# Kernel optimization log

Measured on AMD Instinct MI355X. Metric: run time of the kernel, lower is better.

The kernel has to match this reference:

```python
import jax, jax.numpy as jnp
import numpy as np

N = 200000
K = 16
D = 32
IN_SIZE = K * (K - 1) // 2  # 120
HID = 128


def setup_inputs() -> dict:
    key = jax.random.key(0)
    ks = jax.random.split(key, 12)
    E = N * K
    x = jax.random.normal(ks[0], (N, D), dtype=jnp.float32)
    edge_attr = jax.random.normal(ks[1], (E, D), dtype=jnp.float32)
    # kNN-style edge_index: source node i owns edges [i*K, (i+1)*K)
    src = jnp.repeat(jnp.arange(N, dtype=jnp.int64), K)
    dst = jax.random.randint(ks[2], (E,), 0, N, dtype=jnp.int64)
    edge_index = jnp.stack([src, dst], axis=0)
    s = 0.1
    W1 = jax.random.normal(ks[3], (IN_SIZE, HID), dtype=jnp.float32) * s
    b1 = jnp.zeros((HID,), dtype=jnp.float32)
    W2 = jax.random.normal(ks[4], (HID, HID), dtype=jnp.float32) * s
    b2 = jnp.zeros((HID,), dtype=jnp.float32)
    W3 = jax.random.normal(ks[5], (HID, HID), dtype=jnp.float32) * s
    b3 = jnp.zeros((HID,), dtype=jnp.float32)
    W4 = jax.random.normal(ks[6], (HID, 1), dtype=jnp.float32) * s
    b4 = jnp.zeros((1,), dtype=jnp.float32)
    return {"x": x, "edge_index": edge_index, "edge_attr": edge_attr, "k": K,
            "W1": W1, "b1": b1, "W2": W2, "b2": b2, "W3": W3, "b3": b3,
            "W4": W4, "b4": b4}


def calc_pair_angles(edge_attr, k):
    # edge_attr: [N*k, d] per-edge neighbor vectors, grouped k per node
    E, d = edge_attr.shape
    n = E // k
    v = edge_attr.reshape(n, k, d)
    vn = v / (jnp.linalg.norm(v, axis=-1, keepdims=True) + 1e-12)
    cos = jnp.einsum('nkd,nmd->nkm', vn, vn)  # [n, k, k]
    cos = jnp.clip(cos, -1.0 + 1e-7, 1.0 - 1e-7)
    ang = jnp.arccos(cos)
    iu, ju = jnp.triu_indices(k, 1)
    return ang[:, iu, ju]  # [n, k*(k-1)/2]


def reference(x, edge_index, edge_attr, k, W1, b1, W2, b2, W3, b3, W4, b4):
    # message() returns edge_attr; aggregate() computes pairwise neighbor angles
    feats = calc_pair_angles(edge_attr, k)  # [N, 120]
    h = jnp.tanh(feats @ W1 + b1)
    h = jnp.tanh(h @ W2 + b2)
    h = jnp.tanh(h @ W3 + b3)
    out = jax.nn.sigmoid(h @ W4 + b4)  # [N, 1]
    return out[:, 0]  # squeeze, [N]
```

## Files before the change

kernel.cpp:

```cpp
#include <hip/hip_runtime.h>
#include <hip/hip_bf16.h>
#include <math.h>


#define NTHREADS 256
#define CHUNK    16
#define ASTRIDE  136
#define PBLOCKS  768

typedef _Float16 f16;
typedef f16  f16x8 __attribute__((ext_vector_type(8)));
typedef f16  f16x4 __attribute__((ext_vector_type(4)));
typedef float f32x4 __attribute__((ext_vector_type(4)));

#define MFMA16(a, b, c) __builtin_amdgcn_mfma_f32_16x16x32_f16(a, b, c, 0, 0, 0)

__device__ __forceinline__ float fast_tanh(float x) {
    float e = __expf(2.0f * x);
    return 1.0f - 2.0f * __builtin_amdgcn_rcpf(e + 1.0f);
}

__device__ __forceinline__ float fast_acos(float x) {
    float ax = fabsf(x);
    float p = fmaf(-0.0187293f, ax, 0.0742610f);
    p = fmaf(p, ax, -0.2121144f);
    p = fmaf(p, ax, 1.5707288f);
    float r = sqrtf(1.0f - ax) * p;
    return (x >= 0.0f) ? r : (3.14159265358979f - r);
}

__device__ __forceinline__ void load_lds16(const float* g, float* l) {
    __builtin_amdgcn_global_load_lds(
        (__attribute__((address_space(1))) void*)(g),
        (__attribute__((address_space(3))) void*)(l), 16, 0, 0);
}

__global__ void prep_weights(const float* __restrict__ W1,
                             const float* __restrict__ W2,
                             const float* __restrict__ W3,
                             f16* __restrict__ wt)
{
    int tid = blockIdx.x * 256 + threadIdx.x;
    if (tid >= 3 * 128 * 128) return;
    int layer = tid >> 14;
    int rem   = tid & 16383;
    int j     = rem >> 7;
    int i     = rem & 127;
    const float* W = (layer == 0) ? W1 : ((layer == 1) ? W2 : W3);
    int in_l = (layer == 0) ? 120 : 128;
    float v = (i < in_l) ? W[i * 128 + j] : 0.0f;
    wt[tid] = (f16)v;
}

__global__ __launch_bounds__(NTHREADS, 3)
void gnn_pipe(const float* __restrict__ edge_attr,
              const f16*   __restrict__ wt,
              const float* __restrict__ b1, const float* __restrict__ b2,
              const float* __restrict__ b3,
              const float* __restrict__ W4, const float* __restrict__ b4,
              float* __restrict__ out, int n_nodes, int nchunks)
{
    __shared__ __attribute__((aligned(16))) float stg[8192];
    __shared__ __attribute__((aligned(16))) f16   actA[16 * ASTRIDE];
    __shared__ __attribute__((aligned(16))) f16   actB[16 * ASTRIDE];
    __shared__ __attribute__((aligned(16))) float diag[4][4][16];
    __shared__ __attribute__((aligned(16))) float pbuf[16][4];
    __shared__ __attribute__((aligned(16))) float cbuf[512];

    const int t  = threadIdx.x;
    const int w  = t >> 6;
    const int l  = t & 63;
    const int lr = l & 15;
    const int lg = l >> 4;

    if (t < 128) {
        cbuf[t]       = b1[t];
        cbuf[128 + t] = b2[t];
        cbuf[256 + t] = b3[t];
        cbuf[384 + t] = W4[t];
        actA[(t >> 3) * ASTRIDE + 120 + (t & 7)] = (f16)0.f;
    }
    const float bb4 = b4[0];

    #define LW(L, jj, kt) (*(const f16x8*)(wt + (L) * 16384 + ((w * 2 + (jj)) * 16 + lr) * 128 + (kt) * 32 + lg * 8))
    const f16x8 W000 = LW(0,0,0), W001 = LW(0,0,1), W002 = LW(0,0,2), W003 = LW(0,0,3);
    const f16x8 W010 = LW(0,1,0), W011 = LW(0,1,1), W012 = LW(0,1,2), W013 = LW(0,1,3);
    const f16x8 W100 = LW(1,0,0), W101 = LW(1,0,1), W102 = LW(1,0,2), W103 = LW(1,0,3);
    const f16x8 W110 = LW(1,1,0), W111 = LW(1,1,1), W112 = LW(1,1,2), W113 = LW(1,1,3);
    const f16x8 W200 = LW(2,0,0), W201 = LW(2,0,1), W202 = LW(2,0,2), W203 = LW(2,0,3);
    const f16x8 W210 = LW(2,1,0), W211 = LW(2,1,1), W212 = LW(2,1,2), W213 = LW(2,1,3);
    #undef LW

    const int swsrc = (l * 16) ^ ((l >> 3) << 4);

    #define STAGE(ch_)                                                           \
        {                                                                        \
            const long n0_ = (long)(ch_) * CHUNK + w * 4;                        \
            _Pragma("unroll")                                                    \
            for (int i_ = 0; i_ < 8; ++i_) {                                     \
                long nd_ = n0_ + (i_ >> 1);                                      \
                if (nd_ >= n_nodes) nd_ = n_nodes - 1;                           \
                const float* gs_ = (const float*)((const char*)edge_attr         \
                                   + nd_ * 2048 + (i_ & 1) * 1024 + swsrc);      \
                load_lds16(gs_, &stg[w * 2048 + i_ * 256]);                      \
            }                                                                    \
        }

    #define LBAR()                                                               \
        {                                                                        \
            asm volatile("s_waitcnt lgkmcnt(0)" ::: "memory");                   \
            __builtin_amdgcn_s_barrier();                                        \
            __builtin_amdgcn_sched_barrier(0);                                   \
        }

    #define LAYER(SRC, DST, Wa0, Wa1, Wa2, Wa3, Wb0, Wb1, Wb2, Wb3, BOFF)       \
        {                                                                        \
            const f32x4 BV0 = *(const f32x4*)&cbuf[(BOFF) + (w * 2 + 0) * 16 + lg * 4]; \
            const f32x4 BV1 = *(const f32x4*)&cbuf[(BOFF) + (w * 2 + 1) * 16 + lg * 4]; \
            const f16* sr_ = SRC + lr * ASTRIDE + lg * 8;                        \
            f16x8 s0_ = *(const f16x8*)(sr_);                                    \
            f16x8 s1_ = *(const f16x8*)(sr_ + 32);                               \
            f16x8 s2_ = *(const f16x8*)(sr_ + 64);                               \
            f16x8 s3_ = *(const f16x8*)(sr_ + 96);                               \
            f32x4 a0_ = {0.f, 0.f, 0.f, 0.f}, a1_ = a0_;                         \
            a0_ = MFMA16(Wa0, s0_, a0_); a1_ = MFMA16(Wb0, s0_, a1_);            \
            a0_ = MFMA16(Wa1, s1_, a0_); a1_ = MFMA16(Wb1, s1_, a1_);            \
            a0_ = MFMA16(Wa2, s2_, a0_); a1_ = MFMA16(Wb2, s2_, a1_);            \
            a0_ = MFMA16(Wa3, s3_, a0_); a1_ = MFMA16(Wb3, s3_, a1_);            \
            f16x4 o0_, o1_;                                                      \
            _Pragma("unroll")                                                    \
            for (int r_ = 0; r_ < 4; ++r_) {                                     \
                o0_[r_] = (f16)fast_tanh(a0_[r_] + BV0[r_]);                     \
                o1_[r_] = (f16)fast_tanh(a1_[r_] + BV1[r_]);                     \
            }                                                                    \
            *(f16x4*)(DST + lr * ASTRIDE + (w * 2 + 0) * 16 + lg * 4) = o0_;     \
            *(f16x4*)(DST + lr * ASTRIDE + (w * 2 + 1) * 16 + lg * 4) = o1_;     \
        }

    #define LAYER3(SRC)                                                          \
        {                                                                        \
            const f32x4 bvc0 = *(const f32x4*)&cbuf[256 + (w * 2 + 0) * 16 + lg * 4]; \
            const f32x4 bvc1 = *(const f32x4*)&cbuf[256 + (w * 2 + 1) * 16 + lg * 4]; \
            const f32x4 w4v0 = *(const f32x4*)&cbuf[384 + w * 32 + lg * 4];      \
            const f32x4 w4v1 = *(const f32x4*)&cbuf[384 + w * 32 + 16 + lg * 4]; \
            const f16* sr_ = (SRC) + lr * ASTRIDE + lg * 8;                      \
            f16x8 s0_ = *(const f16x8*)(sr_);                                    \
            f16x8 s1_ = *(const f16x8*)(sr_ + 32);                               \
            f16x8 s2_ = *(const f16x8*)(sr_ + 64);                               \
            f16x8 s3_ = *(const f16x8*)(sr_ + 96);                               \
            f32x4 a0_ = {0.f, 0.f, 0.f, 0.f}, a1_ = a0_;                         \
            a0_ = MFMA16(W200, s0_, a0_); a1_ = MFMA16(W210, s0_, a1_);          \
            a0_ = MFMA16(W201, s1_, a0_); a1_ = MFMA16(W211, s1_, a1_);          \
            a0_ = MFMA16(W202, s2_, a0_); a1_ = MFMA16(W212, s2_, a1_);          \
            a0_ = MFMA16(W203, s3_, a0_); a1_ = MFMA16(W213, s3_, a1_);          \
            float p_ = 0.f;                                                      \
            _Pragma("unroll")                                                    \
            for (int r_ = 0; r_ < 4; ++r_) {                                     \
                p_ = fmaf(fast_tanh(a0_[r_] + bvc0[r_]), w4v0[r_], p_);          \
                p_ = fmaf(fast_tanh(a1_[r_] + bvc1[r_]), w4v1[r_], p_);          \
            }                                                                    \
            p_ += __shfl_xor(p_, 16);                                            \
            p_ += __shfl_xor(p_, 32);                                            \
            if (l < 16) pbuf[lr][w] = p_;                                        \
        }

    #define FINALSUM(ch_)                                                        \
        {                                                                        \
            if (l < 4) {                                                         \
                const int nd_ = w * 4 + l;                                       \
                f32x4 pv_ = *(const f32x4*)&pbuf[nd_][0];                        \
                float s_ = (pv_[0] + pv_[1]) + (pv_[2] + pv_[3]);                \
                const long gn_ = (long)(ch_) * CHUNK + nd_;                      \
                if (gn_ < n_nodes)                                               \
                    out[gn_] = __builtin_amdgcn_rcpf(1.0f + __expf(-(s_ + bb4)));\
            }                                                                    \
        }

    long ch = blockIdx.x;
    STAGE(ch);
    asm volatile("s_waitcnt vmcnt(0)" ::: "memory");
    __builtin_amdgcn_sched_barrier(0);

    int it = 0;
    for (; ch < nchunks; ch += PBLOCKS, ++it) {
        if (it) {
            asm volatile("s_waitcnt vmcnt(1)" ::: "memory");
            __builtin_amdgcn_sched_barrier(0);
        }

        const char* ws_ = (const char*)&stg[w * 2048];
        const int abase = lr * 128 + lg * 32;
        const int akey  = (lr & 7) << 4;
        f16x8 f0, f1, f2, f3;
        #define FRAG(fc, m_)                                                     \
            {                                                                    \
                float4 va = *(const float4*)(ws_ + (m_) * 2048 + (abase ^ akey));        \
                float4 vb = *(const float4*)(ws_ + (m_) * 2048 + ((abase + 16) ^ akey)); \
                fc[0]=(f16)va.x; fc[1]=(f16)va.y; fc[2]=(f16)va.z; fc[3]=(f16)va.w;      \
                fc[4]=(f16)vb.x; fc[5]=(f16)vb.y; fc[6]=(f16)vb.z; fc[7]=(f16)vb.w;      \
            }
        FRAG(f0, 0) FRAG(f1, 1) FRAG(f2, 2) FRAG(f3, 3)
        #undef FRAG

        asm volatile("s_waitcnt lgkmcnt(0)" ::: "memory");
        __builtin_amdgcn_sched_barrier(0);

        const long nxt = ch + PBLOCKS;
        if (nxt < nchunks) STAGE(nxt);

        f32x4 g0, g1, g2, g3;
        {
            f32x4 z = {0.f, 0.f, 0.f, 0.f};
            g0 = MFMA16(f0, f0, z); g1 = MFMA16(f1, f1, z);
            g2 = MFMA16(f2, f2, z); g3 = MFMA16(f3, f3, z);
        }
        if (lg == (lr >> 2)) {
            const int r = lr & 3;
            diag[w][0][lr] = __builtin_amdgcn_rsqf(g0[r] + 1e-24f);
            diag[w][1][lr] = __builtin_amdgcn_rsqf(g1[r] + 1e-24f);
            diag[w][2][lr] = __builtin_amdgcn_rsqf(g2[r] + 1e-24f);
            diag[w][3][lr] = __builtin_amdgcn_rsqf(g3[r] + 1e-24f);
        }
        asm volatile("s_waitcnt lgkmcnt(0)" ::: "memory");
        __builtin_amdgcn_sched_barrier(0);

        #define FIN(gc, c)                                                       \
            {                                                                    \
                const float rc = diag[w][c][lr];                                 \
                const f32x4 rr = *(const f32x4*)&diag[w][c][lg * 4];             \
                const int m_ = w * 4 + (c);                                      \
                const int col = lr;                                              \
                _Pragma("unroll")                                                \
                for (int r2 = 0; r2 < 4; ++r2) {                                 \
                    const int row = lg * 4 + r2;                                 \
                    float cv = gc[r2] * rr[r2] * rc;                             \
                    cv = fminf(fmaxf(cv, -1.0f + 1e-7f), 1.0f - 1e-7f);          \
                    float ang = fast_acos(cv);                                   \
                    if (row < col) {                                             \
                        const int p = 15*row - ((row*(row-1))>>1) + (col-row-1); \
                        actA[m_ * ASTRIDE + p] = (f16)ang;                       \
                    }                                                            \
                }                                                                \
            }
        FIN(g0, 0) FIN(g1, 1) FIN(g2, 2) FIN(g3, 3)
        #undef FIN

        LBAR();

        LAYER(actA, actB, W000, W001, W002, W003, W010, W011, W012, W013, 0);
        LBAR();
        LAYER(actB, actA, W100, W101, W102, W103, W110, W111, W112, W113, 128);
        LBAR();
        LAYER3(actA);
        LBAR();

        FINALSUM(ch);
    }
    #undef STAGE
    #undef LBAR
    #undef LAYER
    #undef LAYER3
    #undef FINALSUM
}

extern "C" void kernel_launch(void* const* d_in, const int* in_sizes, int n_in,
                              void* d_out, int out_size, void* d_ws, size_t ws_size,
                              hipStream_t stream) {
    const float* edge_attr = (const float*)d_in[2];
    const float* W1 = (const float*)d_in[4];
    const float* b1 = (const float*)d_in[5];
    const float* W2 = (const float*)d_in[6];
    const float* b2 = (const float*)d_in[7];
    const float* W3 = (const float*)d_in[8];
    const float* b3 = (const float*)d_in[9];
    const float* W4 = (const float*)d_in[10];
    const float* b4 = (const float*)d_in[11];
    float* out = (float*)d_out;
    f16* wt = (f16*)d_ws;

    const int n_nodes = in_sizes[2] / 512;
    const int nchunks = (n_nodes + CHUNK - 1) / CHUNK;
    const int blocks  = PBLOCKS < nchunks ? PBLOCKS : nchunks;

    prep_weights<<<(3 * 128 * 128 + 255) / 256, 256, 0, stream>>>(W1, W2, W3, wt);

    gnn_pipe<<<blocks, NTHREADS, 0, stream>>>(
        edge_attr, wt, b1, b2, b3, W4, b4, out, n_nodes, nchunks);
}
```

Before: 116.1 us.

## Process two 16-node half-chunks per iteration with interleaved MLP layers

Each loop iteration now handles 32 nodes as two 16-node halves. The MLP layers of the two halves are staggered so that one barrier covers work from both halves, and the next half's global load is issued mid-iteration. The goal is fewer barriers per node and more independent MFMA work between syncs to hide latency. In exchange it uses more LDS for the doubled activation buffers, which may cut occupancy, and adds more complex wait-count bookkeeping.

```diff
diff --git a/kernel.cpp b/kernel.cpp
--- a/kernel.cpp
+++ b/kernel.cpp
@@ -4,9 +4,9 @@
 
 
 #define NTHREADS 256
-#define CHUNK    16
 #define ASTRIDE  136
 #define PBLOCKS  768
+#define S16 (16 * ASTRIDE)
 
 typedef _Float16 f16;
 typedef f16  f16x8 __attribute__((ext_vector_type(8)));
@@ -58,13 +58,13 @@
               const float* __restrict__ b1, const float* __restrict__ b2,
               const float* __restrict__ b3,
               const float* __restrict__ W4, const float* __restrict__ b4,
-              float* __restrict__ out, int n_nodes, int nchunks)
+              float* __restrict__ out, int n_nodes, int nch32)
 {
     __shared__ __attribute__((aligned(16))) float stg[8192];
-    __shared__ __attribute__((aligned(16))) f16   actA[16 * ASTRIDE];
-    __shared__ __attribute__((aligned(16))) f16   actB[16 * ASTRIDE];
+    __shared__ __attribute__((aligned(16))) f16   actA[32 * ASTRIDE];
+    __shared__ __attribute__((aligned(16))) f16   actB[32 * ASTRIDE];
     __shared__ __attribute__((aligned(16))) float diag[4][4][16];
-    __shared__ __attribute__((aligned(16))) float pbuf[16][4];
+    __shared__ __attribute__((aligned(16))) float pbuf[32][4];
     __shared__ __attribute__((aligned(16))) float cbuf[512];
 
     const int t  = threadIdx.x;
@@ -78,7 +78,8 @@
         cbuf[128 + t] = b2[t];
         cbuf[256 + t] = b3[t];
         cbuf[384 + t] = W4[t];
-        actA[(t >> 3) * ASTRIDE + 120 + (t & 7)] = (f16)0.f;
+        actA[(t >> 3) * ASTRIDE + 120 + (t & 7)]        = (f16)0.f;
+        actA[((t >> 3) + 16) * ASTRIDE + 120 + (t & 7)] = (f16)0.f;
     }
     const float bb4 = b4[0];
 
@@ -93,9 +94,9 @@
 
     const int swsrc = (l * 16) ^ ((l >> 3) << 4);
 
-    #define STAGE(ch_)                                                           \
-        {                                                                        \
-            const long n0_ = (long)(ch_) * CHUNK + w * 4;                        \
+    #define STAGE(h_)                                                            \
+        {                                                                        \
+            const long n0_ = (long)(h_) * 16 + w * 4;                            \
             _Pragma("unroll")                                                    \
             for (int i_ = 0; i_ < 8; ++i_) {                                     \
                 long nd_ = n0_ + (i_ >> 1);                                      \
@@ -112,12 +113,69 @@
             __builtin_amdgcn_s_barrier();                                        \
             __builtin_amdgcn_sched_barrier(0);                                   \
         }
+    #define LGKM()                                                               \
+        {                                                                        \
+            asm volatile("s_waitcnt lgkmcnt(0)" ::: "memory");                   \
+            __builtin_amdgcn_sched_barrier(0);                                   \
+        }
+
+    #define FRAGS()                                                              \
+        {                                                                        \
+            const char* ws_ = (const char*)&stg[w * 2048];                       \
+            const int abase = lr * 128 + lg * 32;                                \
+            const int akey  = (lr & 7) << 4;                                     \
+            _FRG(f0, 0) _FRG(f1, 1) _FRG(f2, 2) _FRG(f3, 3)                      \
+        }
+    #define _FRG(fc, m_)                                                         \
+        {                                                                        \
+            float4 va = *(const float4*)(ws_ + (m_) * 2048 + (abase ^ akey));        \
+            float4 vb = *(const float4*)(ws_ + (m_) * 2048 + ((abase + 16) ^ akey)); \
+            fc[0]=(f16)va.x; fc[1]=(f16)va.y; fc[2]=(f16)va.z; fc[3]=(f16)va.w;      \
+            fc[4]=(f16)vb.x; fc[5]=(f16)vb.y; fc[6]=(f16)vb.z; fc[7]=(f16)vb.w;      \
+        }
+
+    #define GRAMFIN(TOFF)                                                        \
+        {                                                                        \
+            f32x4 g0, g1, g2, g3;                                                \
+            {                                                                    \
+                f32x4 z_ = {0.f, 0.f, 0.f, 0.f};                                 \
+                g0 = MFMA16(f0, f0, z_); g1 = MFMA16(f1, f1, z_);                \
+                g2 = MFMA16(f2, f2, z_); g3 = MFMA16(f3, f3, z_);                \
+            }                                                                    \
+            if (lg == (lr >> 2)) {                                               \
+                const int r_ = lr & 3;                                           \
+                diag[w][0][lr] = __builtin_amdgcn_rsqf(g0[r_] + 1e-24f);         \
+                diag[w][1][lr] = __builtin_amdgcn_rsqf(g1[r_] + 1e-24f);         \
+                diag[w][2][lr] = __builtin_amdgcn_rsqf(g2[r_] + 1e-24f);         \
+                diag[w][3][lr] = __builtin_amdgcn_rsqf(g3[r_] + 1e-24f);         \
+            }                                                                    \
+            LGKM();                                                              \
+            _FN(g0, 0, TOFF) _FN(g1, 1, TOFF) _FN(g2, 2, TOFF) _FN(g3, 3, TOFF)  \
+        }
+    #define _FN(gc, c_, TOFF)                                                    \
+        {                                                                        \
+            const float rc = diag[w][c_][lr];                                    \
+            const f32x4 rr = *(const f32x4*)&diag[w][c_][lg * 4];                \
+            const int m_ = (TOFF) + w * 4 + (c_);                                \
+            const int col = lr;                                                  \
+            _Pragma("unroll")                                                    \
+            for (int r2 = 0; r2 < 4; ++r2) {                                     \
+                const int row = lg * 4 + r2;                                     \
+                float cv = gc[r2] * rr[r2] * rc;                                 \
+                cv = fminf(fmaxf(cv, -1.0f + 1e-7f), 1.0f - 1e-7f);              \
+                float ang = fast_acos(cv);                                       \
+                if (row < col) {                                                 \
+                    const int p_ = 15*row - ((row*(row-1))>>1) + (col-row-1);    \
+                    actA[m_ * ASTRIDE + p_] = (f16)ang;                          \
+                }                                                                \
+            }                                                                    \
+        }
 
     #define LAYER(SRC, DST, Wa0, Wa1, Wa2, Wa3, Wb0, Wb1, Wb2, Wb3, BOFF)       \
         {                                                                        \
             const f32x4 BV0 = *(const f32x4*)&cbuf[(BOFF) + (w * 2 + 0) * 16 + lg * 4]; \
             const f32x4 BV1 = *(const f32x4*)&cbuf[(BOFF) + (w * 2 + 1) * 16 + lg * 4]; \
-            const f16* sr_ = SRC + lr * ASTRIDE + lg * 8;                        \
+            const f16* sr_ = (SRC) + lr * ASTRIDE + lg * 8;                      \
             f16x8 s0_ = *(const f16x8*)(sr_);                                    \
             f16x8 s1_ = *(const f16x8*)(sr_ + 32);                               \
             f16x8 s2_ = *(const f16x8*)(sr_ + 64);                               \
@@ -133,11 +191,11 @@
                 o0_[r_] = (f16)fast_tanh(a0_[r_] + BV0[r_]);                     \
                 o1_[r_] = (f16)fast_tanh(a1_[r_] + BV1[r_]);                     \
             }                                                                    \
-            *(f16x4*)(DST + lr * ASTRIDE + (w * 2 + 0) * 16 + lg * 4) = o0_;     \
-            *(f16x4*)(DST + lr * ASTRIDE + (w * 2 + 1) * 16 + lg * 4) = o1_;     \
-        }
-
-    #define LAYER3(SRC)                                                          \
+            *(f16x4*)((DST) + lr * ASTRIDE + (w * 2 + 0) * 16 + lg * 4) = o0_;   \
+            *(f16x4*)((DST) + lr * ASTRIDE + (w * 2 + 1) * 16 + lg * 4) = o1_;   \
+        }
+
+    #define LAYER3(SRC, TOFF)                                                    \
         {                                                                        \
             const f32x4 bvc0 = *(const f32x4*)&cbuf[256 + (w * 2 + 0) * 16 + lg * 4]; \
             const f32x4 bvc1 = *(const f32x4*)&cbuf[256 + (w * 2 + 1) * 16 + lg * 4]; \
@@ -161,103 +219,77 @@
             }                                                                    \
             p_ += __shfl_xor(p_, 16);                                            \
             p_ += __shfl_xor(p_, 32);                                            \
-            if (l < 16) pbuf[lr][w] = p_;                                        \
-        }
-
-    #define FINALSUM(ch_)                                                        \
+            if (l < 16) pbuf[(TOFF) + lr][w] = p_;                               \
+        }
+
+    #define FINALSUM(h_, TOFF)                                                   \
         {                                                                        \
             if (l < 4) {                                                         \
-                const int nd_ = w * 4 + l;                                       \
-                f32x4 pv_ = *(const f32x4*)&pbuf[nd_][0];                        \
+                const int r_ = w * 4 + l;                                        \
+                f32x4 pv_ = *(const f32x4*)&pbuf[(TOFF) + r_][0];                \
                 float s_ = (pv_[0] + pv_[1]) + (pv_[2] + pv_[3]);                \
-                const long gn_ = (long)(ch_) * CHUNK + nd_;                      \
+                const long gn_ = (long)(h_) * 16 + r_;                           \
                 if (gn_ < n_nodes)                                               \
                     out[gn_] = __builtin_amdgcn_rcpf(1.0f + __expf(-(s_ + bb4)));\
             }                                                                    \
         }
 
     long ch = blockIdx.x;
-    STAGE(ch);
+    STAGE(2 * ch);
     asm volatile("s_waitcnt vmcnt(0)" ::: "memory");
     __builtin_amdgcn_sched_barrier(0);
 
-    int it = 0;
-    for (; ch < nchunks; ch += PBLOCKS, ++it) {
+    long lastB = -1;
+    for (int it = 0; ch < nch32; ch += PBLOCKS, ++it) {
+        const long hA = 2 * ch, hB = 2 * ch + 1;
+        f16x8 f0, f1, f2, f3;
+
         if (it) {
             asm volatile("s_waitcnt vmcnt(1)" ::: "memory");
             __builtin_amdgcn_sched_barrier(0);
-        }
-
-        const char* ws_ = (const char*)&stg[w * 2048];
-        const int abase = lr * 128 + lg * 32;
-        const int akey  = (lr & 7) << 4;
-        f16x8 f0, f1, f2, f3;
-        #define FRAG(fc, m_)                                                     \
-            {                                                                    \
-                float4 va = *(const float4*)(ws_ + (m_) * 2048 + (abase ^ akey));        \
-                float4 vb = *(const float4*)(ws_ + (m_) * 2048 + ((abase + 16) ^ akey)); \
-                fc[0]=(f16)va.x; fc[1]=(f16)va.y; fc[2]=(f16)va.z; fc[3]=(f16)va.w;      \
-                fc[4]=(f16)vb.x; fc[5]=(f16)vb.y; fc[6]=(f16)vb.z; fc[7]=(f16)vb.w;      \
-            }
-        FRAG(f0, 0) FRAG(f1, 1) FRAG(f2, 2) FRAG(f3, 3)
-        #undef FRAG
-
-        asm volatile("s_waitcnt lgkmcnt(0)" ::: "memory");
+            FINALSUM(lastB, 16);
+        }
+        FRAGS();
+        LGKM();
+        STAGE(hB);
+        GRAMFIN(0);
+        LBAR();
+
+        LAYER(actA, actB, W000, W001, W002, W003, W010, W011, W012, W013, 0);
+        asm volatile("s_waitcnt vmcnt(0)" ::: "memory");
         __builtin_amdgcn_sched_barrier(0);
-
-        const long nxt = ch + PBLOCKS;
-        if (nxt < nchunks) STAGE(nxt);
-
-        f32x4 g0, g1, g2, g3;
+        FRAGS();
+        LGKM();
         {
-            f32x4 z = {0.f, 0.f, 0.f, 0.f};
-            g0 = MFMA16(f0, f0, z); g1 = MFMA16(f1, f1, z);
-            g2 = MFMA16(f2, f2, z); g3 = MFMA16(f3, f3, z);
-        }
-        if (lg == (lr >> 2)) {
-            const int r = lr & 3;
-            diag[w][0][lr] = __builtin_amdgcn_rsqf(g0[r] + 1e-24f);
-            diag[w][1][lr] = __builtin_amdgcn_rsqf(g1[r] + 1e-24f);
-            diag[w][2][lr] = __builtin_amdgcn_rsqf(g2[r] + 1e-24f);
-            diag[w][3][lr] = __builtin_amdgcn_rsqf(g3[r] + 1e-24f);
-        }
-        asm volatile("s_waitcnt lgkmcnt(0)" ::: "memory");
-        __builtin_amdgcn_sched_barrier(0);
-
-        #define FIN(gc, c)                                                       \
-            {                                                                    \
-                const float rc = diag[w][c][lr];                                 \
-                const f32x4 rr = *(const f32x4*)&diag[w][c][lg * 4];             \
-                const int m_ = w * 4 + (c);                                      \
-                const int col = lr;                                              \
-                _Pragma("unroll")                                                \
-                for (int r2 = 0; r2 < 4; ++r2) {                                 \
-                    const int row = lg * 4 + r2;                                 \
-                    float cv = gc[r2] * rr[r2] * rc;                             \
-                    cv = fminf(fmaxf(cv, -1.0f + 1e-7f), 1.0f - 1e-7f);          \
-                    float ang = fast_acos(cv);                                   \
-                    if (row < col) {                                             \
-                        const int p = 15*row - ((row*(row-1))>>1) + (col-row-1); \
-                        actA[m_ * ASTRIDE + p] = (f16)ang;                       \
-                    }                                                            \
-                }                                                                \
-            }
-        FIN(g0, 0) FIN(g1, 1) FIN(g2, 2) FIN(g3, 3)
-        #undef FIN
-
-        LBAR();
-
-        LAYER(actA, actB, W000, W001, W002, W003, W010, W011, W012, W013, 0);
-        LBAR();
+            const long nc = ch + PBLOCKS;
+            if (nc < nch32) STAGE(2 * nc);
+        }
+        GRAMFIN(16);
+        LBAR();
+
         LAYER(actB, actA, W100, W101, W102, W103, W110, W111, W112, W113, 128);
-        LBAR();
-        LAYER3(actA);
-        LBAR();
-
-        FINALSUM(ch);
+        LAYER(actA + S16, actB + S16, W000, W001, W002, W003, W010, W011, W012, W013, 0);
+        LBAR();
+
+        LAYER3(actA, 0);
+        LAYER(actB + S16, actA + S16, W100, W101, W102, W103, W110, W111, W112, W113, 128);
+        LBAR();
+
+        FINALSUM(hA, 0);
+        LAYER3(actA + S16, 16);
+        LBAR();
+
+        lastB = hB;
     }
+    if (lastB >= 0) FINALSUM(lastB, 16);
+
     #undef STAGE
     #undef LBAR
+    #undef LGKM
+    #undef FRAGS
+    #undef _FRG
+    #undef GRAMFIN
+    #undef _FN
     #undef LAYER
     #undef LAYER3
     #undef FINALSUM
@@ -279,11 +311,11 @@
     f16* wt = (f16*)d_ws;
 
     const int n_nodes = in_sizes[2] / 512;
-    const int nchunks = (n_nodes + CHUNK - 1) / CHUNK;
-    const int blocks  = PBLOCKS < nchunks ? PBLOCKS : nchunks;
+    const int nch32   = (n_nodes + 31) / 32;
+    const int blocks  = PBLOCKS < nch32 ? PBLOCKS : nch32;
 
     prep_weights<<<(3 * 128 * 128 + 255) / 256, 256, 0, stream>>>(W1, W2, W3, wt);
 
     gnn_pipe<<<blocks, NTHREADS, 0, stream>>>(
-        edge_attr, wt, b1, b2, b3, W4, b4, out, n_nodes, nchunks);
-}
+        edge_attr, wt, b1, b2, b3, W4, b4, out, n_nodes, nch32);
+}
```

Result: slower. 130.2 us (+12.2%).
